# Kernel optimization log

Hardware: AMD Instinct MI355X
Metric: run time of the kernel (lower is better)

Reference implementation:

```python
import jax, jax.numpy as jnp
import numpy as np

B, C, H, W = 8, 512, 48, 48
K = 4
MID = C // K  # 128
EPS = 1e-5  # BatchNorm eps; running_mean=0, running_var=1 (eval-mode BN)


def conv1x1(x, Wt, b):
    # x: [B,C,H,W], Wt: [out,in], b: [out]
    return jnp.einsum('bchw,mc->bmhw', x, Wt) + b[None, :, None, None]


def bn_relu(y, gamma, beta):
    # eval BN with mean=0, var=1
    return jax.nn.relu(y * (gamma / jnp.sqrt(1.0 + EPS))[None, :, None, None]
                       + beta[None, :, None, None])


def setup_inputs() -> dict:
    key = jax.random.key(0)
    ks = jax.random.split(key, 24)
    s = 0.05
    n = lambda k, shape, sc=1.0: jax.random.normal(k, shape, dtype=jnp.float32) * sc
    return {
        'x':   n(ks[0], (B, C, H, W)),
        'x_h': n(ks[1], (B, C, H, W)),
        'x_v': n(ks[2], (B, C, H, W)),
        # f_a: conv1x1 + BN + ReLU
        'Wa': n(ks[3], (MID, C), s), 'ba': n(ks[4], (MID,), s),
        'ga': jnp.ones((MID,), jnp.float32) + n(ks[5], (MID,), s), 'ta': n(ks[6], (MID,), s),
        # f_v: conv1x1 + BN + ReLU (also applied to x_h, as in original code)
        'Wv': n(ks[7], (MID, C), s), 'bv': n(ks[8], (MID,), s),
        'gv': jnp.ones((MID,), jnp.float32) + n(ks[9], (MID,), s), 'tv': n(ks[10], (MID,), s),
        # g_av, g_ah: plain conv1x1
        'Wgav': n(ks[11], (MID, C), s), 'bgav': n(ks[12], (MID,), s),
        'Wgah': n(ks[13], (MID, C), s), 'bgah': n(ks[14], (MID,), s),
        # f_av, f_ah: output conv1x1 (mid -> in_ch)
        'Wfav': n(ks[15], (C, MID), s), 'bfav': n(ks[16], (C,), s),
        'Wfah': n(ks[17], (C, MID), s), 'bfah': n(ks[18], (C,), s),
    }


def reference(x, x_h, x_v, Wa, ba, ga, ta, Wv, bv, gv, tv,
              Wgav, bgav, Wgah, bgah, Wfav, bfav, Wfah, bfah):
    N = H * W
    f_a = bn_relu(conv1x1(x,   Wa, ba), ga, ta).reshape(B, MID, N)
    f_v = bn_relu(conv1x1(x_v, Wv, bv), gv, tv).reshape(B, MID, N)
    # NOTE: original forward applies self.f_v to x_h (f_h module unused)
    f_h = bn_relu(conv1x1(x_h, Wv, bv), gv, tv).reshape(B, MID, N)

    scale = MID ** (-0.5)
    # [B,N,N] attention: queries from f_v/f_h, keys from f_a, softmax over last dim
    A_av = jax.nn.softmax(scale * jnp.einsum('bmi,bmj->bij', f_v, f_a), axis=-1)
    A_ah = jax.nn.softmax(scale * jnp.einsum('bmi,bmj->bij', f_h, f_a), axis=-1)

    g_av = conv1x1(x, Wgav, bgav).reshape(B, MID, N)
    g_ah = conv1x1(x, Wgah, bgah).reshape(B, MID, N)

    o_v = jnp.einsum('bmn,bnj->bmj', g_av, A_av).reshape(B, MID, H, W)
    o_v = conv1x1(o_v, Wfav, bfav) + x
    o_h = jnp.einsum('bmn,bnj->bmj', g_ah, A_ah).reshape(B, MID, H, W)
    o_h = conv1x1(o_h, Wfah, bfah) + x
    return (o_h, o_v)
```

## Files before the change

kernel.cpp:

```cpp
#include <hip/hip_runtime.h>


typedef __attribute__((ext_vector_type(8))) short short8;
typedef __attribute__((ext_vector_type(4))) short short4_t;
typedef __attribute__((ext_vector_type(8))) __bf16 bf16x8;
typedef __attribute__((ext_vector_type(4))) float f32x4;

#define DEV __device__ __forceinline__

constexpr int BB = 8, CC = 512, MID = 128, NB = 2304;
constexpr float ATT_SCALE = 0.08838834764831845f;
constexpr float RSQ = 0.9999950000374998f;

DEV float bf2f(unsigned short u) {
    unsigned int x = ((unsigned int)u) << 16;
    return __builtin_bit_cast(float, x);
}
DEV unsigned short f2bf(float f) {
    unsigned int x = __builtin_bit_cast(unsigned int, f);
    x += 0x7fffu + ((x >> 16) & 1u);
    return (unsigned short)(x >> 16);
}
DEV bf16x8 ldfrag(const unsigned short* p) {
    return __builtin_bit_cast(bf16x8, *(const short8*)p);
}

__global__ __launch_bounds__(256)
void fold_kernel(const float* __restrict__ Wa, const float* __restrict__ ba,
                 const float* __restrict__ ga, const float* __restrict__ ta,
                 const float* __restrict__ Wv, const float* __restrict__ bv,
                 const float* __restrict__ gv, const float* __restrict__ tv,
                 const float* __restrict__ Wgav, const float* __restrict__ bgav,
                 const float* __restrict__ Wgah, const float* __restrict__ bgah,
                 const float* __restrict__ Wfav, const float* __restrict__ bfav,
                 const float* __restrict__ Wfah, const float* __restrict__ bfah,
                 unsigned short* __restrict__ WaE, unsigned short* __restrict__ WvE,
                 unsigned short* __restrict__ WgavE, unsigned short* __restrict__ WgahE,
                 unsigned short* __restrict__ WfavE, unsigned short* __restrict__ WfahE,
                 float* __restrict__ biases)
{
    int idx = blockIdx.x * 256 + threadIdx.x;
    if (idx < 65536) {
        int m = idx >> 9;
        WaE[idx]   = f2bf(ga[m] * RSQ * Wa[idx]);
        WvE[idx]   = f2bf(gv[m] * RSQ * Wv[idx]);
        WgavE[idx] = f2bf(Wgav[idx]);
        WgahE[idx] = f2bf(Wgah[idx]);
        WfavE[idx] = f2bf(Wfav[idx]);
        WfahE[idx] = f2bf(Wfah[idx]);
    }
    if (idx < 128) {
        biases[idx]       = ba[idx] * ga[idx] * RSQ + ta[idx];
        biases[128 + idx] = bv[idx] * gv[idx] * RSQ + tv[idx];
        biases[256 + idx] = bgav[idx];
        biases[384 + idx] = bgah[idx];
    }
    if (idx < 512) {
        biases[512 + idx]  = bfav[idx];
        biases[1024 + idx] = bfah[idx];
    }
}

template<bool AT, int EPI, bool BF32, bool OF32, bool EXPB>
__global__ __launch_bounds__(256)
void gemm_kernel(const unsigned short* __restrict__ A, long sAb,
                 const void* __restrict__ Bm, long sBb,
                 void* __restrict__ Out, long sOb,
                 const float* __restrict__ bias,
                 const float* __restrict__ resid, long sRb,
                 const float* __restrict__ stats,
                 int Mdim, int Kdim, int Ndim, float outscale)
{
    constexpr int TM = 64, TN = 64, TK = 32, LD = TK + 8;
    __shared__ unsigned short As[TM * LD];
    __shared__ unsigned short Bs[TN * LD];

    const int tid  = threadIdx.x;
    const int lane = tid & 63;
    const int wave = tid >> 6;
    const int wm = wave >> 1, wn = wave & 1;
    const int m0 = blockIdx.y * TM, n0 = blockIdx.x * TN;
    const int z  = blockIdx.z;

    const unsigned short* Ab = A + (long)z * sAb;

    f32x4 acc[2][2] = {};

    const int ar = tid >> 2, ac = (tid & 3) * 8;
    const int tk = tid >> 3, tq = (tid & 7) * 8;
    const int lm = lane & 15, kq = (lane >> 4) * 8;

    for (int k0 = 0; k0 < Kdim; k0 += TK) {
        if constexpr (!AT) {
            short8 v = *(const short8*)(Ab + (long)(m0 + ar) * Kdim + (k0 + ac));
            *(short8*)(&As[ar * LD + ac]) = v;
        } else {
            short8 v = *(const short8*)(Ab + (long)(k0 + tk) * Mdim + (m0 + tq));
            #pragma unroll
            for (int i = 0; i < 8; i++) As[(tq + i) * LD + tk] = (unsigned short)v[i];
        }
        if constexpr (BF32) {
            const float* Bf = (const float*)Bm + (long)z * sBb;
            f32x4 a0 = *(const f32x4*)(Bf + (long)(k0 + tk) * Ndim + (n0 + tq));
            f32x4 a1 = *(const f32x4*)(Bf + (long)(k0 + tk) * Ndim + (n0 + tq) + 4);
            #pragma unroll
            for (int i = 0; i < 4; i++) Bs[(tq + i) * LD + tk]     = f2bf(a0[i]);
            #pragma unroll
            for (int i = 0; i < 4; i++) Bs[(tq + 4 + i) * LD + tk] = f2bf(a1[i]);
        } else {
            const unsigned short* Bu = (const unsigned short*)Bm + (long)z * sBb;
            short8 v = *(const short8*)(Bu + (long)(k0 + tk) * Ndim + (n0 + tq));
            if constexpr (EXPB) {
                const long krow = (long)z * NB + (k0 + tk);
                const float mrow = stats[2 * krow];
                const float rinv = stats[2 * krow + 1];
                #pragma unroll
                for (int i = 0; i < 8; i++)
                    Bs[(tq + i) * LD + tk] =
                        f2bf(__expf(bf2f((unsigned short)v[i]) - mrow) * rinv);
            } else {
                #pragma unroll
                for (int i = 0; i < 8; i++) Bs[(tq + i) * LD + tk] = (unsigned short)v[i];
            }
        }
        __syncthreads();

        bf16x8 afr[2], bfr[2];
        afr[0] = __builtin_bit_cast(bf16x8, *(const short8*)(&As[(wm * 32 + lm) * LD + kq]));
        afr[1] = __builtin_bit_cast(bf16x8, *(const short8*)(&As[(wm * 32 + 16 + lm) * LD + kq]));
        bfr[0] = __builtin_bit_cast(bf16x8, *(const short8*)(&Bs[(wn * 32 + lm) * LD + kq]));
        bfr[1] = __builtin_bit_cast(bf16x8, *(const short8*)(&Bs[(wn * 32 + 16 + lm) * LD + kq]));
        #pragma unroll
        for (int i = 0; i < 2; i++)
            #pragma unroll
            for (int j = 0; j < 2; j++)
                acc[i][j] = __builtin_amdgcn_mfma_f32_16x16x32_bf16(afr[i], bfr[j], acc[i][j], 0, 0, 0);
        __syncthreads();
    }

    const float* Rb = nullptr;
    if constexpr (EPI == 3) Rb = resid + (long)z * sRb;

    const int col = lane & 15, rb = (lane >> 4) * 4;
    #pragma unroll
    for (int i = 0; i < 2; i++) {
        #pragma unroll
        for (int j = 0; j < 2; j++) {
            const int mB = m0 + wm * 32 + i * 16 + rb;
            const int on = n0 + wn * 32 + j * 16 + col;
            #pragma unroll
            for (int r = 0; r < 4; r++) {
                const int m = mB + r;
                float v = acc[i][j][r];
                if constexpr (EPI == 0) {
                    v *= outscale;
                } else {
                    v += bias[m];
                    if constexpr (EPI == 1) v = fmaxf(v, 0.0f);
                    if constexpr (EPI == 3) v += Rb[(long)m * Ndim + on];
                }
                if constexpr (OF32) {
                    float* Of = (float*)Out + (long)z * sOb;
                    Of[(long)m * Ndim + on] = v;
                } else {
                    unsigned short* Ou = (unsigned short*)Out + (long)z * sOb;
                    Ou[(long)m * Ndim + on] = f2bf(v);
                }
            }
        }
    }
}

__global__ __launch_bounds__(256)
void proj4_kernel(const unsigned short* __restrict__ W0, const unsigned short* __restrict__ W1,
                  const unsigned short* __restrict__ W2, const unsigned short* __restrict__ W3,
                  const float* __restrict__ b0, const float* __restrict__ b1,
                  const float* __restrict__ b2, const float* __restrict__ b3,
                  const float* __restrict__ S0, const float* __restrict__ S1,
                  const float* __restrict__ S2, const float* __restrict__ S3,
                  unsigned short* __restrict__ D0, unsigned short* __restrict__ D1,
                  unsigned short* __restrict__ D2, unsigned short* __restrict__ D3,
                  int reluMask)
{
    constexpr int TK = 32, LD = TK + 8;
    const long sF = (long)MID * NB, sX = (long)CC * NB;
    const int zz = blockIdx.z, cls = zz >> 3, b = zz & 7;
    const unsigned short* W = cls == 0 ? W0 : cls == 1 ? W1 : cls == 2 ? W2 : W3;
    const float* bi = cls == 0 ? b0 : cls == 1 ? b1 : cls == 2 ? b2 : b3;
    const float* Bf = (cls == 0 ? S0 : cls == 1 ? S1 : cls == 2 ? S2 : S3) + (long)b * sX;
    unsigned short* outp = (cls == 0 ? D0 : cls == 1 ? D1 : cls == 2 ? D2 : D3) + (long)b * sF;
    const bool relu = (reluMask >> cls) & 1;

    __shared__ unsigned short As[64 * LD];
    __shared__ unsigned short Bs[64 * LD];

    const int tid = threadIdx.x, lane = tid & 63, wave = tid >> 6;
    const int wm = wave >> 1, wn = wave & 1;
    const int m0 = blockIdx.y * 64, n0 = blockIdx.x * 64;
    const int ar = tid >> 2, ac = (tid & 3) * 8;
    const int tk = tid >> 3, tq = (tid & 7) * 8;
    const int lm = lane & 15, kq = (lane >> 4) * 8;

    f32x4 acc[2][2] = {};
    for (int k0 = 0; k0 < CC; k0 += TK) {
        short8 v = *(const short8*)(W + (long)(m0 + ar) * CC + (k0 + ac));
        *(short8*)(&As[ar * LD + ac]) = v;
        f32x4 a0 = *(const f32x4*)(Bf + (long)(k0 + tk) * NB + (n0 + tq));
        f32x4 a1 = *(const f32x4*)(Bf + (long)(k0 + tk) * NB + (n0 + tq) + 4);
        #pragma unroll
        for (int i = 0; i < 4; i++) Bs[(tq + i) * LD + tk]     = f2bf(a0[i]);
        #pragma unroll
        for (int i = 0; i < 4; i++) Bs[(tq + 4 + i) * LD + tk] = f2bf(a1[i]);
        __syncthreads();
        bf16x8 afr[2], bfr[2];
        afr[0] = ldfrag(&As[(wm * 32 + lm) * LD + kq]);
        afr[1] = ldfrag(&As[(wm * 32 + 16 + lm) * LD + kq]);
        bfr[0] = ldfrag(&Bs[(wn * 32 + lm) * LD + kq]);
        bfr[1] = ldfrag(&Bs[(wn * 32 + 16 + lm) * LD + kq]);
        #pragma unroll
        for (int i = 0; i < 2; i++)
            #pragma unroll
            for (int j = 0; j < 2; j++)
                acc[i][j] = __builtin_amdgcn_mfma_f32_16x16x32_bf16(afr[i], bfr[j], acc[i][j], 0, 0, 0);
        __syncthreads();
    }

    const int col = lane & 15, rb = (lane >> 4) * 4;
    #pragma unroll
    for (int i = 0; i < 2; i++) {
        #pragma unroll
        for (int j = 0; j < 2; j++) {
            const int mB = m0 + wm * 32 + i * 16 + rb;
            const int on = n0 + wn * 32 + j * 16 + col;
            #pragma unroll
            for (int r = 0; r < 4; r++) {
                const int m = mB + r;
                float v = acc[i][j][r] + bi[m];
                if (relu) v = fmaxf(v, 0.0f);
                outp[(long)m * NB + on] = f2bf(v);
            }
        }
    }
}

__global__ __launch_bounds__(256)
void transpose_kernel(const unsigned short* __restrict__ src,
                      unsigned short* __restrict__ dst)
{
    constexpr int LT = 72;
    const long sF = (long)MID * NB;
    const int b = blockIdx.z;
    const unsigned short* s = src + (long)b * sF;
    unsigned short* d = dst + (long)b * sF;
    const int n0 = blockIdx.x * 64, m0 = blockIdx.y * 64;
    const int tid = threadIdx.x;
    const int tk = tid >> 3, tq = (tid & 7) * 8;

    __shared__ unsigned short T[64 * LT];

    #pragma unroll
    for (int mm = 0; mm < 64; mm += 32) {
        short8 v = *(const short8*)(s + (long)(m0 + mm + tk) * NB + n0 + tq);
        #pragma unroll
        for (int e = 0; e < 8; e++) T[(tq + e) * LT + mm + tk] = (unsigned short)v[e];
    }
    __syncthreads();
    #pragma unroll
    for (int rr = 0; rr < 2; rr++) {
        int c = rr * 256 + tid;
        int nr = c >> 3, mc = (c & 7) * 8;
        *(short8*)(d + (long)(n0 + nr) * MID + m0 + mc) = *(const short8*)(&T[nr * LT + mc]);
    }
}

__global__ __launch_bounds__(256)
void scoreT_kernel(const unsigned short* __restrict__ faT,
                   const unsigned short* __restrict__ fqT,
                   unsigned short* __restrict__ PT,
                   float* __restrict__ sums)
{
    constexpr int LD = 40;
    const long sF = (long)MID * NB, sP = (long)NB * NB;
    const int z = blockIdx.z;
    const unsigned short* Ab = faT + (long)z * sF;
    const unsigned short* Bb = fqT + (long)z * sF;
    unsigned short* Ou = PT + (long)z * sP;
    float* sm = sums + (long)z * NB;

    __shared__ unsigned short As[64 * LD];
    __shared__ unsigned short Bs[64 * LD];

    const int tid = threadIdx.x, lane = tid & 63, wave = tid >> 6;
    const int wm = wave >> 1, wn = wave & 1;
    const int m0 = blockIdx.y * 64, n0 = blockIdx.x * 64;
    const int ar = tid >> 2, ac = (tid & 3) * 8;
    const int lm = lane & 15, kq = (lane >> 4) * 8;

    f32x4 acc[2][2] = {};
    #pragma unroll
    for (int k0 = 0; k0 < MID; k0 += 32) {
        *(short8*)(&As[ar * LD + ac]) = *(const short8*)(Ab + (long)(m0 + ar) * MID + (k0 + ac));
        *(short8*)(&Bs[ar * LD + ac]) = *(const short8*)(Bb + (long)(n0 + ar) * MID + (k0 + ac));
        __syncthreads();
        bf16x8 afr[2], bfr[2];
        afr[0] = ldfrag(&As[(wm * 32 + lm) * LD + kq]);
        afr[1] = ldfrag(&As[(wm * 32 + 16 + lm) * LD + kq]);
        bfr[0] = ldfrag(&Bs[(wn * 32 + lm) * LD + kq]);
        bfr[1] = ldfrag(&Bs[(wn * 32 + 16 + lm) * LD + kq]);
        #pragma unroll
        for (int i = 0; i < 2; i++)
            #pragma unroll
            for (int j = 0; j < 2; j++)
                acc[i][j] = __builtin_amdgcn_mfma_f32_16x16x32_bf16(afr[i], bfr[j], acc[i][j], 0, 0, 0);
        __syncthreads();
    }

    const int col = lane & 15, rb = (lane >> 4) * 4;
    float csum[2] = {0.f, 0.f};
    #pragma unroll
    for (int i = 0; i < 2; i++) {
        #pragma unroll
        for (int j = 0; j < 2; j++) {
            const int mB = m0 + wm * 32 + i * 16 + rb;
            const int on = n0 + wn * 32 + j * 16 + col;
            #pragma unroll
            for (int r = 0; r < 4; r++) {
                unsigned short u = f2bf(acc[i][j][r] * ATT_SCALE);
                Ou[(long)(mB + r) * NB + on] = u;
                csum[j] += __expf(bf2f(u));
            }
        }
    }
    csum[0] += __shfl_xor(csum[0], 16, 64);
    csum[0] += __shfl_xor(csum[0], 32, 64);
    csum[1] += __shfl_xor(csum[1], 16, 64);
    csum[1] += __shfl_xor(csum[1], 32, 64);
    if (lane < 16) {
        atomicAdd(&sm[n0 + wn * 32 + lane],      csum[0]);
        atomicAdd(&sm[n0 + wn * 32 + 16 + lane], csum[1]);
    }
}

__global__ __launch_bounds__(256)
void stats_inv_kernel(float* __restrict__ p)
{
    int idx = blockIdx.x * 256 + threadIdx.x;
    if (idx < BB * NB) p[idx] = 1.0f / p[idx];
}

__global__ __launch_bounds__(256)
void pv2_kernel(const unsigned short* __restrict__ g,
                const unsigned short* __restrict__ PT,
                const float* __restrict__ rinv,
                float* __restrict__ omidF)
{
    constexpr int TK = 32, LD = TK + 8;
    const long sF = (long)MID * NB, sP = (long)NB * NB;
    const int zb = blockIdx.z / 3, zs = blockIdx.z % 3;
    const unsigned short* Ab = g + (long)zb * sF;
    const unsigned short* Bt = PT + (long)zb * sP;
    const float* rv = rinv + (long)zb * NB;
    float* Of = omidF + (long)zb * sF;

    __shared__ unsigned short As[64 * LD];
    __shared__ unsigned short Bs[64 * LD];

    const int tid = threadIdx.x, lane = tid & 63, wave = tid >> 6;
    const int wm = wave >> 1, wn = wave & 1;
    const int m0 = blockIdx.y * 64, n0 = blockIdx.x * 64;
    const int ar = tid >> 2, ac = (tid & 3) * 8;
    const int lm = lane & 15, kq = (lane >> 4) * 8;

    f32x4 acc[2][2] = {};
    const int kBeg = zs * 768, kEnd = kBeg + 768;
    for (int k0 = kBeg; k0 < kEnd; k0 += TK) {
        *(short8*)(&As[ar * LD + ac]) = *(const short8*)(Ab + (long)(m0 + ar) * NB + (k0 + ac));
        {
            short8 v = *(const short8*)(Bt + (long)(n0 + ar) * NB + (k0 + ac));
            f32x4 r0 = *(const f32x4*)(rv + k0 + ac);
            f32x4 r1 = *(const f32x4*)(rv + k0 + ac + 4);
            short8 w;
            #pragma unroll
            for (int e = 0; e < 4; e++)
                w[e] = (short)f2bf(__expf(bf2f((unsigned short)v[e])) * r0[e]);
            #pragma unroll
            for (int e = 0; e < 4; e++)
                w[4 + e] = (short)f2bf(__expf(bf2f((unsigned short)v[4 + e])) * r1[e]);
            *(short8*)(&Bs[ar * LD + ac]) = w;
        }
        __syncthreads();

        bf16x8 afr[2], bfr[2];
        afr[0] = ldfrag(&As[(wm * 32 + lm) * LD + kq]);
        afr[1] = ldfrag(&As[(wm * 32 + 16 + lm) * LD + kq]);
        bfr[0] = ldfrag(&Bs[(wn * 32 + lm) * LD + kq]);
        bfr[1] = ldfrag(&Bs[(wn * 32 + 16 + lm) * LD + kq]);
        #pragma unroll
        for (int i = 0; i < 2; i++)
            #pragma unroll
            for (int j = 0; j < 2; j++)
                acc[i][j] = __builtin_amdgcn_mfma_f32_16x16x32_bf16(afr[i], bfr[j], acc[i][j], 0, 0, 0);
        __syncthreads();
    }

    const int col = lane & 15, rb = (lane >> 4) * 4;
    #pragma unroll
    for (int i = 0; i < 2; i++)
        #pragma unroll
        for (int j = 0; j < 2; j++) {
            const int mB = m0 + wm * 32 + i * 16 + rb;
            const int on = n0 + wn * 32 + j * 16 + col;
            #pragma unroll
            for (int r = 0; r < 4; r++)
                atomicAdd(&Of[(long)(mB + r) * NB + on], acc[i][j][r]);
        }
}

__global__ __launch_bounds__(256)
void zerof_kernel(float* __restrict__ p, int n)
{
    int stride = gridDim.x * 256;
    for (int i = blockIdx.x * 256 + threadIdx.x; i < n; i += stride) p[i] = 0.0f;
}

__global__ __launch_bounds__(256)
void softmax_rows(unsigned short* __restrict__ P)
{
    const int row  = blockIdx.x * 4 + (threadIdx.x >> 6);
    const int lane = threadIdx.x & 63;
    unsigned short* p = P + (long)row * NB;

    float vals[36];
    #pragma unroll
    for (int c = 0; c < 4; c++) {
        short8 v = *(const short8*)(p + c * 512 + lane * 8);
        #pragma unroll
        for (int e = 0; e < 8; e++) vals[c * 8 + e] = bf2f((unsigned short)v[e]);
    }
    {
        short4_t v = *(const short4_t*)(p + 2048 + lane * 4);
        #pragma unroll
        for (int e = 0; e < 4; e++) vals[32 + e] = bf2f((unsigned short)v[e]);
    }

    float mx = vals[0];
    #pragma unroll
    for (int i = 1; i < 36; i++) mx = fmaxf(mx, vals[i]);
    #pragma unroll
    for (int off = 32; off > 0; off >>= 1) mx = fmaxf(mx, __shfl_xor(mx, off, 64));

    float s = 0.f;
    #pragma unroll
    for (int i = 0; i < 36; i++) { vals[i] = __expf(vals[i] - mx); s += vals[i]; }
    #pragma unroll
    for (int off = 32; off > 0; off >>= 1) s += __shfl_xor(s, off, 64);
    const float rs = 1.0f / s;

    #pragma unroll
    for (int c = 0; c < 4; c++) {
        short8 w;
        #pragma unroll
        for (int e = 0; e < 8; e++) w[e] = (short)f2bf(vals[c * 8 + e] * rs);
        *(short8*)(p + c * 512 + lane * 8) = w;
    }
    {
        short4_t w;
        #pragma unroll
        for (int e = 0; e < 4; e++) w[e] = (short)f2bf(vals[32 + e] * rs);
        *(short4_t*)(p + 2048 + lane * 4) = w;
    }
}

extern "C" void kernel_launch(void* const* d_in, const int* in_sizes, int n_in,
                              void* d_out, int out_size, void* d_ws, size_t ws_size,
                              hipStream_t stream)
{
    const float* x    = (const float*)d_in[0];
    const float* x_h  = (const float*)d_in[1];
    const float* x_v  = (const float*)d_in[2];
    const float* Wa   = (const float*)d_in[3];
    const float* ba   = (const float*)d_in[4];
    const float* ga   = (const float*)d_in[5];
    const float* ta   = (const float*)d_in[6];
    const float* Wv   = (const float*)d_in[7];
    const float* bv   = (const float*)d_in[8];
    const float* gv   = (const float*)d_in[9];
    const float* tv   = (const float*)d_in[10];
    const float* Wgav = (const float*)d_in[11];
    const float* bgav = (const float*)d_in[12];
    const float* Wgah = (const float*)d_in[13];
    const float* bgah = (const float*)d_in[14];
    const float* Wfav = (const float*)d_in[15];
    const float* bfav = (const float*)d_in[16];
    const float* Wfah = (const float*)d_in[17];
    const float* bfah = (const float*)d_in[18];
    float* out = (float*)d_out;

    const long sX = (long)CC * NB;
    const long sF = (long)MID * NB;
    const long sP = (long)NB * NB;
    const long HALF = (long)BB * sX;

    const dim3 blk(256);
    unsigned short* ws = (unsigned short*)d_ws;

    constexpr size_t WS_BIG = 114112512ull;

    if (ws_size >= WS_BIG) {
        unsigned short* WaE   = ws;
        unsigned short* WvE   = ws + 65536;
        unsigned short* WgavE = ws + 131072;
        unsigned short* WgahE = ws + 196608;
        unsigned short* WfavE = ws + 262144;
        unsigned short* WfahE = ws + 327680;
        float* biases = (float*)(ws + 393216);
        float* rinv   = (float*)(ws + 396288);
        unsigned short* fa   = ws + 433152;
        unsigned short* faT  = ws + 2792448;
        unsigned short* gav  = ws + 5151744;
        unsigned short* gah  = ws + 7511040;
        unsigned short* fq   = ws + 9870336;
        unsigned short* fqT  = ws + 12229632;
        float* omidF         = (float*)(ws + 9870336);
        unsigned short* PT   = ws + 14588928;

        float* baE   = biases;
        float* bvE   = biases + 128;
        float* bgavF = biases + 256;
        float* bgahF = biases + 384;
        float* bfavF = biases + 512;
        float* bfahF = biases + 1024;

        fold_kernel<<<256, 256, 0, stream>>>(Wa, ba, ga, ta, Wv, bv, gv, tv,
                                             Wgav, bgav, Wgah, bgah, Wfav, bfav, Wfah, bfah,
                                             WaE, WvE, WgavE, WgahE, WfavE, WfahE, biases);

        proj4_kernel<<<dim3(36, 2, 32), blk, 0, stream>>>(
            WaE, WvE, WgavE, WgahE,
            baE, bvE, bgavF, bgahF,
            x, x_v, x, x,
            fa, fq, gav, gah, 3);

        transpose_kernel<<<dim3(36, 2, 8), blk, 0, stream>>>(fa, faT);
        transpose_kernel<<<dim3(36, 2, 8), blk, 0, stream>>>(fq, fqT);

        zerof_kernel<<<72, blk, 0, stream>>>(rinv, BB * NB);
        scoreT_kernel<<<dim3(36, 36, 8), blk, 0, stream>>>(faT, fqT, PT, rinv);
        stats_inv_kernel<<<72, blk, 0, stream>>>(rinv);
        zerof_kernel<<<1024, blk, 0, stream>>>(omidF, (int)(BB * sF));
        pv2_kernel<<<dim3(36, 2, 24), blk, 0, stream>>>(gav, PT, rinv, omidF);
        gemm_kernel<false,3,true,true,false><<<dim3(36,8,8), blk, 0, stream>>>(
            WfavE, 0, omidF, sF, out + HALF, sX, bfavF, x, sX, nullptr, CC, MID, NB, 1.f);

        proj4_kernel<<<dim3(36, 2, 8), blk, 0, stream>>>(
            WvE, WvE, WvE, WvE,
            bvE, bvE, bvE, bvE,
            x_h, x_h, x_h, x_h,
            fq, fq, fq, fq, 1);
        transpose_kernel<<<dim3(36, 2, 8), blk, 0, stream>>>(fq, fqT);

        zerof_kernel<<<72, blk, 0, stream>>>(rinv, BB * NB);
        scoreT_kernel<<<dim3(36, 36, 8), blk, 0, stream>>>(faT, fqT, PT, rinv);
        stats_inv_kernel<<<72, blk, 0, stream>>>(rinv);
        zerof_kernel<<<1024, blk, 0, stream>>>(omidF, (int)(BB * sF));
        pv2_kernel<<<dim3(36, 2, 24), blk, 0, stream>>>(gah, PT, rinv, omidF);
        gemm_kernel<false,3,true,true,false><<<dim3(36,8,8), blk, 0, stream>>>(
            WfahE, 0, omidF, sF, out, sX, bfahF, x, sX, nullptr, CC, MID, NB, 1.f);

        return;
    }

    constexpr size_t WS_NEED = 7280640;
    if (ws_size < WS_NEED) return;

    unsigned short* WaE   = ws;
    unsigned short* WvE   = ws + 65536;
    unsigned short* WgavE = ws + 131072;
    unsigned short* WgahE = ws + 196608;
    unsigned short* WfavE = ws + 262144;
    unsigned short* WfahE = ws + 327680;
    float* biases = (float*)(ws + 393216);
    unsigned short* fab  = ws + 396288;
    unsigned short* qb   = ws + 691200;
    unsigned short* gb   = ws + 986112;
    unsigned short* omid = ws + 1281024;
    unsigned short* Pb = (unsigned short*)d_out;

    float* baE   = biases;
    float* bvE   = biases + 128;
    float* bgavF = biases + 256;
    float* bgahF = biases + 384;
    float* bfavF = biases + 512;
    float* bfahF = biases + 1024;

    fold_kernel<<<256, 256, 0, stream>>>(Wa, ba, ga, ta, Wv, bv, gv, tv,
                                         Wgav, bgav, Wgah, bgah, Wfav, bfav, Wfah, bfah,
                                         WaE, WvE, WgavE, WgahE, WfavE, WfahE, biases);

    for (int b = 0; b < BB; b++) {
        const float* xb  = x   + (long)b * sX;
        const float* xqb = x_v + (long)b * sX;
        gemm_kernel<false,1,true,false,false><<<dim3(36,2,1), blk, 0, stream>>>(WaE,   0, xb,  0, fab, 0, baE,   nullptr, 0, nullptr, MID, CC, NB, 1.f);
        gemm_kernel<false,1,true,false,false><<<dim3(36,2,1), blk, 0, stream>>>(WvE,   0, xqb, 0, qb,  0, bvE,   nullptr, 0, nullptr, MID, CC, NB, 1.f);
        gemm_kernel<false,2,true,false,false><<<dim3(36,2,1), blk, 0, stream>>>(WgavE, 0, xb,  0, gb,  0, bgavF, nullptr, 0, nullptr, MID, CC, NB, 1.f);
        gemm_kernel<true,0,false,false,false><<<dim3(36,36,1), blk, 0, stream>>>(qb, 0, fab, 0, Pb, 0, nullptr, nullptr, 0, nullptr, NB, MID, NB, ATT_SCALE);
        softmax_rows<<<NB / 4, blk, 0, stream>>>(Pb);
        gemm_kernel<false,0,false,false,false><<<dim3(36,2,1), blk, 0, stream>>>(gb, 0, Pb, 0, omid + (long)b * sF, 0, nullptr, nullptr, 0, nullptr, MID, NB, NB, 1.f);
    }
    gemm_kernel<false,3,false,true,false><<<dim3(36,8,8), blk, 0, stream>>>(WfavE, 0, omid, sF, out + HALF, sX, bfavF, x, sX, nullptr, CC, MID, NB, 1.f);

    for (int b = 0; b < BB; b++) {
        const float* xb  = x   + (long)b * sX;
        const float* xqb = x_h + (long)b * sX;
        gemm_kernel<false,1,true,false,false><<<dim3(36,2,1), blk, 0, stream>>>(WaE,   0, xb,  0, fab, 0, baE,   nullptr, 0, nullptr, MID, CC, NB, 1.f);
        gemm_kernel<false,1,true,false,false><<<dim3(36,2,1), blk, 0, stream>>>(WvE,   0, xqb, 0, qb,  0, bvE,   nullptr, 0, nullptr, MID, CC, NB, 1.f);
        gemm_kernel<false,2,true,false,false><<<dim3(36,2,1), blk, 0, stream>>>(WgahE, 0, xb,  0, gb,  0, bgahF, nullptr, 0, nullptr, MID, CC, NB, 1.f);
        gemm_kernel<true,0,false,false,false><<<dim3(36,36,1), blk, 0, stream>>>(qb, 0, fab, 0, Pb, 0, nullptr, nullptr, 0, nullptr, NB, MID, NB, ATT_SCALE);
        softmax_rows<<<NB / 4, blk, 0, stream>>>(Pb);
        gemm_kernel<false,0,false,false,false><<<dim3(36,2,1), blk, 0, stream>>>(gb, 0, Pb, 0, omid + (long)b * sF, 0, nullptr, nullptr, 0, nullptr, MID, NB, NB, 1.f);
    }
    gemm_kernel<false,3,false,true,false><<<dim3(36,8,8), blk, 0, stream>>>(WfahE, 0, omid, sF, out, sX, bfahF, x, sX, nullptr, CC, MID, NB, 1.f);

    (void)in_sizes; (void)n_in; (void)out_size;
}
```

Measured before the change: 476.8 us.

## Pre-cast inputs to transposed bf16 once and feed projections from bf16

```diff
diff --git a/kernel.cpp b/kernel.cpp
--- a/kernel.cpp
+++ b/kernel.cpp
@@ -172,12 +172,56 @@
 }
 
 __global__ __launch_bounds__(256)
-void proj4_kernel(const unsigned short* __restrict__ W0, const unsigned short* __restrict__ W1,
+void castT_kernel(const float* __restrict__ src, unsigned short* __restrict__ dst)
+{
+    const long sX = (long)CC * NB;
+    const int b = blockIdx.z;
+    const float* s = src + (long)b * sX;
+    unsigned short* d = dst + (long)b * sX;
+    const int n0 = blockIdx.x * 64, c0 = blockIdx.y * 64;
+    const int t = threadIdx.x;
+
+    __shared__ unsigned int T32[64 * 33];
+
+    #pragma unroll
+    for (int r = 0; r < 2; r++) {
+        const int cp = (t >> 4) + 16 * r;
+        const int nb = (t & 15) * 4;
+        const int c  = c0 + 2 * cp;
+        f32x4 v0 = *(const f32x4*)(s + (long)c * NB + n0 + nb);
+        f32x4 v1 = *(const f32x4*)(s + (long)(c + 1) * NB + n0 + nb);
+        #pragma unroll
+        for (int i = 0; i < 4; i++) {
+            unsigned int u = (unsigned int)f2bf(v0[i]) |
+                             ((unsigned int)f2bf(v1[i]) << 16);
+            T32[(nb + i) * 33 + cp] = u;
+        }
+    }
+    __syncthreads();
+    #pragma unroll
+    for (int rr = 0; rr < 2; rr++) {
+        const int nr = (t >> 3) + 32 * rr;
+        const int mc = (t & 7) * 8;
+        unsigned int q[4];
+        #pragma unroll
+        for (int j = 0; j < 4; j++) q[j] = T32[nr * 33 + (mc >> 1) + j];
+        short8 w;
+        #pragma unroll
+        for (int j = 0; j < 4; j++) {
+            w[2 * j]     = (short)(q[j] & 0xffffu);
+            w[2 * j + 1] = (short)(q[j] >> 16);
+        }
+        *(short8*)(d + (long)(n0 + nr) * CC + c0 + mc) = w;
+    }
+}
+
+__global__ __launch_bounds__(256)
+void projb_kernel(const unsigned short* __restrict__ W0, const unsigned short* __restrict__ W1,
                   const unsigned short* __restrict__ W2, const unsigned short* __restrict__ W3,
                   const float* __restrict__ b0, const float* __restrict__ b1,
                   const float* __restrict__ b2, const float* __restrict__ b3,
-                  const float* __restrict__ S0, const float* __restrict__ S1,
-                  const float* __restrict__ S2, const float* __restrict__ S3,
+                  const unsigned short* __restrict__ X0, const unsigned short* __restrict__ X1,
+                  const unsigned short* __restrict__ X2, const unsigned short* __restrict__ X3,
                   unsigned short* __restrict__ D0, unsigned short* __restrict__ D1,
                   unsigned short* __restrict__ D2, unsigned short* __restrict__ D3,
                   int reluMask)
@@ -187,7 +231,7 @@
     const int zz = blockIdx.z, cls = zz >> 3, b = zz & 7;
     const unsigned short* W = cls == 0 ? W0 : cls == 1 ? W1 : cls == 2 ? W2 : W3;
     const float* bi = cls == 0 ? b0 : cls == 1 ? b1 : cls == 2 ? b2 : b3;
-    const float* Bf = (cls == 0 ? S0 : cls == 1 ? S1 : cls == 2 ? S2 : S3) + (long)b * sX;
+    const unsigned short* Xt = (cls == 0 ? X0 : cls == 1 ? X1 : cls == 2 ? X2 : X3) + (long)b * sX;
     unsigned short* outp = (cls == 0 ? D0 : cls == 1 ? D1 : cls == 2 ? D2 : D3) + (long)b * sF;
     const bool relu = (reluMask >> cls) & 1;
 
@@ -198,19 +242,12 @@
     const int wm = wave >> 1, wn = wave & 1;
     const int m0 = blockIdx.y * 64, n0 = blockIdx.x * 64;
     const int ar = tid >> 2, ac = (tid & 3) * 8;
-    const int tk = tid >> 3, tq = (tid & 7) * 8;
     const int lm = lane & 15, kq = (lane >> 4) * 8;
 
     f32x4 acc[2][2] = {};
     for (int k0 = 0; k0 < CC; k0 += TK) {
-        short8 v = *(const short8*)(W + (long)(m0 + ar) * CC + (k0 + ac));
-        *(short8*)(&As[ar * LD + ac]) = v;
-        f32x4 a0 = *(const f32x4*)(Bf + (long)(k0 + tk) * NB + (n0 + tq));
-        f32x4 a1 = *(const f32x4*)(Bf + (long)(k0 + tk) * NB + (n0 + tq) + 4);
-        #pragma unroll
-        for (int i = 0; i < 4; i++) Bs[(tq + i) * LD + tk]     = f2bf(a0[i]);
-        #pragma unroll
-        for (int i = 0; i < 4; i++) Bs[(tq + 4 + i) * LD + tk] = f2bf(a1[i]);
+        *(short8*)(&As[ar * LD + ac]) = *(const short8*)(W  + (long)(m0 + ar) * CC + (k0 + ac));
+        *(short8*)(&Bs[ar * LD + ac]) = *(const short8*)(Xt + (long)(n0 + ar) * CC + (k0 + ac));
         __syncthreads();
         bf16x8 afr[2], bfr[2];
         afr[0] = ldfrag(&As[(wm * 32 + lm) * LD + kq]);
@@ -516,13 +553,15 @@
         float* biases = (float*)(ws + 393216);
         float* rinv   = (float*)(ws + 396288);
         unsigned short* fa   = ws + 433152;
-        unsigned short* faT  = ws + 2792448;
-        unsigned short* gav  = ws + 5151744;
-        unsigned short* gah  = ws + 7511040;
-        unsigned short* fq   = ws + 9870336;
+        unsigned short* fv   = ws + 2792448;
+        float* omidF         = (float*)(ws + 433152);
+        unsigned short* faT  = ws + 5151744;
+        unsigned short* gav  = ws + 7511040;
+        unsigned short* gah  = ws + 9870336;
         unsigned short* fqT  = ws + 12229632;
-        float* omidF         = (float*)(ws + 9870336);
         unsigned short* PT   = ws + 14588928;
+        unsigned short* slotA = PT;
+        unsigned short* slotB = PT + 9437184;
 
         float* baE   = biases;
         float* bvE   = biases + 128;
@@ -535,14 +574,17 @@
                                              Wgav, bgav, Wgah, bgah, Wfav, bfav, Wfah, bfah,
                                              WaE, WvE, WgavE, WgahE, WfavE, WfahE, biases);
 
-        proj4_kernel<<<dim3(36, 2, 32), blk, 0, stream>>>(
+        castT_kernel<<<dim3(36, 8, 8), blk, 0, stream>>>(x,   slotA);
+        castT_kernel<<<dim3(36, 8, 8), blk, 0, stream>>>(x_v, slotB);
+
+        projb_kernel<<<dim3(36, 2, 32), blk, 0, stream>>>(
             WaE, WvE, WgavE, WgahE,
             baE, bvE, bgavF, bgahF,
-            x, x_v, x, x,
-            fa, fq, gav, gah, 3);
+            slotA, slotB, slotA, slotA,
+            fa, fv, gav, gah, 3);
 
         transpose_kernel<<<dim3(36, 2, 8), blk, 0, stream>>>(fa, faT);
-        transpose_kernel<<<dim3(36, 2, 8), blk, 0, stream>>>(fq, fqT);
+        transpose_kernel<<<dim3(36, 2, 8), blk, 0, stream>>>(fv, fqT);
 
         zerof_kernel<<<72, blk, 0, stream>>>(rinv, BB * NB);
         scoreT_kernel<<<dim3(36, 36, 8), blk, 0, stream>>>(faT, fqT, PT, rinv);
@@ -552,12 +594,13 @@
         gemm_kernel<false,3,true,true,false><<<dim3(36,8,8), blk, 0, stream>>>(
             WfavE, 0, omidF, sF, out + HALF, sX, bfavF, x, sX, nullptr, CC, MID, NB, 1.f);
 
-        proj4_kernel<<<dim3(36, 2, 8), blk, 0, stream>>>(
+        castT_kernel<<<dim3(36, 8, 8), blk, 0, stream>>>(x_h, slotA);
+        projb_kernel<<<dim3(36, 2, 8), blk, 0, stream>>>(
             WvE, WvE, WvE, WvE,
             bvE, bvE, bvE, bvE,
-            x_h, x_h, x_h, x_h,
-            fq, fq, fq, fq, 1);
-        transpose_kernel<<<dim3(36, 2, 8), blk, 0, stream>>>(fq, fqT);
+            slotA, slotA, slotA, slotA,
+            gav, gav, gav, gav, 1);
+        transpose_kernel<<<dim3(36, 2, 8), blk, 0, stream>>>(gav, fqT);
 
         zerof_kernel<<<72, blk, 0, stream>>>(rinv, BB * NB);
         scoreT_kernel<<<dim3(36, 36, 8), blk, 0, stream>>>(faT, fqT, PT, rinv);
```

Result: no change. 477.6 us (+0.2%).
